# Kernel optimization log

Measured on AMD Instinct MI355X. Metric: run time of the kernel, lower is better.

Reference implementation:

```python
import jax, jax.numpy as jnp
import numpy as np

N = 100000
E = 1600000
D_IN = 256
D_OUT = 128
ALPHA = 0.2  # LeakyReLU negative slope


def setup_inputs() -> dict:
    key = jax.random.key(0)
    k1, k2, k3, k4, k5 = jax.random.split(key, 5)
    x = jax.random.normal(k1, (N, D_IN), dtype=jnp.float32)
    # random edges + self-loops so every destination row has >=1 incoming edge
    src = jax.random.randint(k2, (E - N,), 0, N)
    dst = jax.random.randint(k3, (E - N,), 0, N)
    loops = jnp.arange(N)
    edge = jnp.stack([jnp.concatenate([src, loops]),
                      jnp.concatenate([dst, loops])]).astype(jnp.int64)  # [2, E]
    W = jax.random.normal(k4, (D_IN, D_OUT), dtype=jnp.float32) * 0.1
    a = jax.random.normal(k5, (1, 2 * D_OUT), dtype=jnp.float32) * 0.1
    return {"x": x, "edge": edge, "W": W, "a": a}


def reference(x, edge, W, a):
    n = x.shape[0]
    d_out = W.shape[1]
    h = x @ W  # [n, d_out]
    src, dst = edge[0], edge[1]
    # a @ concat(h[src], h[dst]) decomposes into two per-node projections
    f_src = h @ a[0, :d_out]   # [n]
    f_dst = h @ a[0, d_out:]   # [n]
    tmp = f_src[src] + f_dst[dst]                      # [E]
    lrelu = jnp.where(tmp > 0, tmp, ALPHA * tmp)
    edge_e = jnp.exp(-lrelu)                           # [E]
    # spmm(A, ones) -> rowsum; spmm(A, h) -> weighted aggregation (rows = src)
    e_rowsum = jax.ops.segment_sum(edge_e, src, num_segments=n)           # [n]
    hh = jax.ops.segment_sum(edge_e[:, None] * h[dst], src, num_segments=n)  # [n, d_out]
    hh = hh / e_rowsum[:, None]
    return jax.nn.elu(hh)  # end=False -> apply ELU
```

## Files before the change

### kernel.cpp

```cpp
#include <hip/hip_runtime.h>

#define D_IN 256
#define D_OUT 128
#define ALPHA 0.2f
#define RB 64
#define RBSH 6
#define NBMAX 1600
#define CH 8192
#define CAPG 1536
#define OVFCAP 32768
#define LKH 128
#define BM 64

typedef __attribute__((ext_vector_type(8))) short bf16x8;
typedef __attribute__((ext_vector_type(4))) float f32x4;

__device__ inline unsigned short f2bf(float f) {
    unsigned int u = __float_as_uint(f);
    return (unsigned short)((u + 0x7FFFu + ((u >> 16) & 1u)) >> 16);
}
__device__ inline float bf2f(unsigned short u) {
    return __uint_as_float(((unsigned int)u) << 16);
}
__device__ inline unsigned int cvt_pk_bf16(float lo, float hi) {
    unsigned int r;
    asm("v_cvt_pk_bf16_f32 %0, %1, %2" : "=v"(r) : "v"(lo), "v"(hi));
    return r;
}

__global__ __launch_bounds__(256) void k_wt(const float* __restrict__ W,
                                            unsigned short* __restrict__ WTb) {
    const int ncol = blockIdx.x;
    const int k = threadIdx.x;
    WTb[(size_t)ncol * 256 + k] = f2bf(W[(size_t)k * 128 + ncol]);
}

__global__ __launch_bounds__(256) void k_fused(const float* __restrict__ x,
                                               const unsigned short* __restrict__ WTb,
                                               const float* __restrict__ a,
                                               unsigned short* __restrict__ hb,
                                               float* __restrict__ f_src,
                                               float* __restrict__ f_dst, int n,
                                               const int* __restrict__ src,
                                               const int* __restrict__ dst,
                                               int* __restrict__ gcnt,
                                               int2* __restrict__ ovf,
                                               int* __restrict__ gkeys, int E, int nb,
                                               int nbf) {
    __shared__ char smem[BM * LKH * 2];
    __shared__ float sFp[BM][2][2];
    const int t = threadIdx.x;

    if (blockIdx.x < nbf) {
        int* cnt = (int*)smem;
        int* bas = cnt + NBMAX;
        const int e0 = blockIdx.x * CH;
        const int e1 = min(e0 + CH, E);
        for (int i = t; i < nb; i += 256) cnt[i] = 0;
        __syncthreads();
        for (int e = e0 + t; e < e1; e += 256) atomicAdd(&cnt[src[e] >> RBSH], 1);
        __syncthreads();
        for (int b = t; b < nb; b += 256) {
            int c = cnt[b];
            bas[b] = c ? atomicAdd(&gcnt[b], c) : 0;
            cnt[b] = 0;
        }
        __syncthreads();
        for (int e = e0 + t; e < e1; e += 256) {
            int s = src[e], d = dst[e];
            int b = s >> RBSH;
            int key = ((s & (RB - 1)) << 17) | d;
            int r = bas[b] + atomicAdd(&cnt[b], 1);
            if (r < CAPG) {
                gkeys[b * CAPG + r] = key;
            } else {
                int o = atomicAdd(&gcnt[nb], 1);
                if (o < OVFCAP) ovf[o] = make_int2(b, key);
            }
        }
        return;
    }

    unsigned short* sA = (unsigned short*)smem;
    const int l = t & 63;
    const int w = t >> 6;
    const int wr = w >> 1, wc = w & 1;
    const int row0 = (blockIdx.x - nbf) * BM;
    const int col0 = wc * 64;
    const int lr = l & 15;
    const int g = l >> 4;
    const int lk8 = g * 8;

    f32x4 acc[2][4] = {};
    const unsigned short* bp[4];
    #pragma unroll
    for (int ni = 0; ni < 4; ++ni)
        bp[ni] = WTb + (size_t)(col0 + ni * 16 + lr) * 256 + lk8;

    #pragma unroll
    for (int half = 0; half < 2; ++half) {
        {
            const int rr = t >> 4;
            const int cc = (t & 15) * 8;
            #pragma unroll
            for (int it = 0; it < 4; ++it) {
                int r = it * 16 + rr;
                int gr = row0 + r;
                float4 fa, fb;
                if (gr < n) {
                    const float* xp = &x[(size_t)gr * D_IN + half * LKH + cc];
                    fa = *(const float4*)xp;
                    fb = *(const float4*)(xp + 4);
                } else {
                    fa = make_float4(0.f, 0.f, 0.f, 0.f);
                    fb = fa;
                }
                uint4 v;
                v.x = cvt_pk_bf16(fa.x, fa.y);
                v.y = cvt_pk_bf16(fa.z, fa.w);
                v.z = cvt_pk_bf16(fb.x, fb.y);
                v.w = cvt_pk_bf16(fb.z, fb.w);
                int js = (cc >> 3) ^ ((r & 7) << 1);
                *(uint4*)&sA[r * LKH + js * 8] = v;
            }
        }
        __syncthreads();

        #pragma unroll
        for (int k0 = 0; k0 < LKH; k0 += 32) {
            bf16x8 af[2], bfr[4];
            #pragma unroll
            for (int mi = 0; mi < 2; ++mi) {
                int row_l = wr * 32 + mi * 16 + lr;
                int js = ((k0 >> 3) + g) ^ ((row_l & 7) << 1);
                af[mi] = *(const bf16x8*)&sA[row_l * LKH + js * 8];
            }
            #pragma unroll
            for (int ni = 0; ni < 4; ++ni)
                bfr[ni] = *(const bf16x8*)(bp[ni] + half * LKH + k0);
            #pragma unroll
            for (int mi = 0; mi < 2; ++mi)
                #pragma unroll
                for (int ni = 0; ni < 4; ++ni)
                    acc[mi][ni] = __builtin_amdgcn_mfma_f32_16x16x32_bf16(
                        af[mi], bfr[ni], acc[mi][ni], 0, 0, 0);
        }
        __syncthreads();
    }

    #pragma unroll
    for (int mi = 0; mi < 2; ++mi) {
        #pragma unroll
        for (int q = 0; q < 4; ++q) {
            int r = row0 + wr * 32 + mi * 16 + g * 4 + q;
            if (r < n) {
                unsigned int a01 = cvt_pk_bf16(acc[mi][0][q], acc[mi][1][q]);
                unsigned int a23 = cvt_pk_bf16(acc[mi][2][q], acc[mi][3][q]);
                unsigned short* hp = &hb[(size_t)r * D_OUT + col0 + lr];
                hp[0]  = (unsigned short)(a01 & 0xFFFF);
                hp[16] = (unsigned short)(a01 >> 16);
                hp[32] = (unsigned short)(a23 & 0xFFFF);
                hp[48] = (unsigned short)(a23 >> 16);
            }
        }
    }

    float asv[4], adv[4];
    #pragma unroll
    for (int ni = 0; ni < 4; ++ni) {
        asv[ni] = a[col0 + ni * 16 + lr];
        adv[ni] = a[D_OUT + col0 + ni * 16 + lr];
    }
    #pragma unroll
    for (int mi = 0; mi < 2; ++mi) {
        #pragma unroll
        for (int q = 0; q < 4; ++q) {
            float fs = 0.f, fd = 0.f;
            #pragma unroll
            for (int ni = 0; ni < 4; ++ni) {
                float v = acc[mi][ni][q];
                fs = fmaf(v, asv[ni], fs);
                fd = fmaf(v, adv[ni], fd);
            }
            #pragma unroll
            for (int m = 1; m < 16; m <<= 1) {
                fs += __shfl_xor(fs, m);
                fd += __shfl_xor(fd, m);
            }
            if (lr == 0) {
                int rl = wr * 32 + mi * 16 + g * 4 + q;
                sFp[rl][wc][0] = fs;
                sFp[rl][wc][1] = fd;
            }
        }
    }
    __syncthreads();
    if (t < BM) {
        int r = row0 + t;
        if (r < n) {
            f_src[r] = sFp[t][0][0] + sFp[t][1][0];
            f_dst[r] = sFp[t][0][1] + sFp[t][1][1];
        }
    }
}

__global__ __launch_bounds__(512, 8) void k_bagg(const unsigned short* __restrict__ hb,
                                                 const float* __restrict__ f_src,
                                                 const float* __restrict__ f_dst,
                                                 const int* __restrict__ gcnt,
                                                 const int2* __restrict__ ovf,
                                                 const int* __restrict__ gkeys,
                                                 float* __restrict__ out, int n, int nb) {
    __shared__ int2 sdw[CAPG];
    __shared__ int nbase[RB];
    __shared__ int ncnt[RB];
    __shared__ int ncur[RB];
    __shared__ float fsl[RB];
    __shared__ int sc[RB];
    const int t = threadIdx.x;
    const int b = blockIdx.x;
    const int s0 = b * RB;
    const int nn = min(RB, n - s0);
    const int beg = b * CAPG;
    const int stored = min(gcnt[b], CAPG);
    const int ovf_n = min(gcnt[nb], OVFCAP);

    for (int i = t; i < RB; i += 512) {
        ncnt[i] = 0;
        fsl[i] = (i < nn) ? f_src[s0 + i] : 0.f;
    }
    __syncthreads();

    for (int i = t; i < stored; i += 512)
        atomicAdd(&ncnt[gkeys[beg + i] >> 17], 1);
    __syncthreads();

    if (t < RB) sc[t] = ncnt[t];
    __syncthreads();
    for (int off = 1; off < RB; off <<= 1) {
        int v = 0;
        if (t < RB && t >= off) v = sc[t - off];
        __syncthreads();
        if (t < RB) sc[t] += v;
        __syncthreads();
    }
    if (t < RB) {
        nbase[t] = sc[t] - ncnt[t];
        ncur[t]  = sc[t] - ncnt[t];
    }
    __syncthreads();

    for (int i = t; i < stored; i += 512) {
        int k = gkeys[beg + i];
        int d = k & 0x1FFFF, ls = k >> 17;
        float tmp = fsl[ls] + f_dst[d];
        float w = __expf(-((tmp > 0.f) ? tmp : ALPHA * tmp));
        int pos = atomicAdd(&ncur[ls], 1);
        sdw[pos] = make_int2(d, __float_as_int(w));
    }
    __syncthreads();

    const int lane = t & 63, wid = t >> 6;
    const int cl = (lane & 31) * 4;
    const bool isB = lane >= 32;
    for (int ni = wid; ni < nn; ni += 8) {
        const int jb = nbase[ni];
        const int cn = ncnt[ni];
        const int halfA = (cn + 1) >> 1;
        const int halfB = cn - halfA;
        const int lim = isB ? halfB : halfA;
        const int jbh = jb + (isB ? halfA : 0);
        float a0 = 0.f, a1 = 0.f, a2 = 0.f, a3 = 0.f, rowsum = 0.f;
        #pragma unroll 4
        for (int it = 0; it < halfA; ++it) {
            bool valid = it < lim;
            int2 dw = sdw[valid ? (jbh + it) : jb];
            float w = valid ? __int_as_float(dw.y) : 0.f;
            ushort4 hv = *(const ushort4*)&hb[(size_t)dw.x * D_OUT + cl];
            rowsum += w;
            a0 = fmaf(w, bf2f(hv.x), a0);
            a1 = fmaf(w, bf2f(hv.y), a1);
            a2 = fmaf(w, bf2f(hv.z), a2);
            a3 = fmaf(w, bf2f(hv.w), a3);
        }
        if (ovf_n > 0) {
            for (int o = 0; o < ovf_n; ++o) {
                int2 ov = ovf[o];
                if (ov.x == b && (ov.y >> 17) == ni && !isB) {
                    int d = ov.y & 0x1FFFF;
                    float tmp = fsl[ni] + f_dst[d];
                    float w = __expf(-((tmp > 0.f) ? tmp : ALPHA * tmp));
                    ushort4 hv = *(const ushort4*)&hb[(size_t)d * D_OUT + cl];
                    rowsum += w;
                    a0 = fmaf(w, bf2f(hv.x), a0);
                    a1 = fmaf(w, bf2f(hv.y), a1);
                    a2 = fmaf(w, bf2f(hv.z), a2);
                    a3 = fmaf(w, bf2f(hv.w), a3);
                }
            }
        }
        rowsum += __shfl_xor(rowsum, 32);
        a0 += __shfl_xor(a0, 32);
        a1 += __shfl_xor(a1, 32);
        a2 += __shfl_xor(a2, 32);
        a3 += __shfl_xor(a3, 32);
        if (!isB) {
            float inv = 1.f / rowsum;
            a0 *= inv; a1 *= inv; a2 *= inv; a3 *= inv;
            a0 = (a0 > 0.f) ? a0 : (__expf(a0) - 1.f);
            a1 = (a1 > 0.f) ? a1 : (__expf(a1) - 1.f);
            a2 = (a2 > 0.f) ? a2 : (__expf(a2) - 1.f);
            a3 = (a3 > 0.f) ? a3 : (__expf(a3) - 1.f);
            *(float4*)&out[(size_t)(s0 + ni) * D_OUT + cl] =
                make_float4(a0, a1, a2, a3);
        }
    }
}

extern "C" void kernel_launch(void* const* d_in, const int* in_sizes, int n_in,
                              void* d_out, int out_size, void* d_ws, size_t ws_size,
                              hipStream_t stream) {
    const float* x    = (const float*)d_in[0];
    const int*   edge = (const int*)d_in[1];
    const float* W    = (const float*)d_in[2];
    const float* a    = (const float*)d_in[3];
    float* out = (float*)d_out;

    const int n = in_sizes[0] / D_IN;
    const int E = in_sizes[1] / 2;
    const int* src = edge;
    const int* dst = edge + E;
    const int nb = (n + RB - 1) / RB;

    char* p = (char*)d_ws;
    unsigned short* hb  = (unsigned short*)p; p += (size_t)n * D_OUT * sizeof(unsigned short);
    unsigned short* WTb = (unsigned short*)p; p += (size_t)D_OUT * D_IN * sizeof(unsigned short);
    float* f_src = (float*)p;  p += (size_t)n * sizeof(float);
    float* f_dst = (float*)p;  p += (size_t)n * sizeof(float);
    int*  gcnt   = (int*)p;    p += (size_t)(nb + 1) * sizeof(int);
    int2* ovf    = (int2*)p;   p += (size_t)OVFCAP * sizeof(int2);
    int*  gkeys  = (int*)p;    p += (size_t)nb * CAPG * sizeof(int);

    const int gemm_blocks = (n + BM - 1) / BM;
    const int nbf = (E + CH - 1) / CH;

    hipMemsetAsync(gcnt, 0, (size_t)(nb + 1) * sizeof(int), stream);
    k_wt<<<D_OUT, 256, 0, stream>>>(W, WTb);
    k_fused<<<nbf + gemm_blocks, 256, 0, stream>>>(x, WTb, a, hb, f_src, f_dst, n,
                                                   src, dst, gcnt, ovf, gkeys, E, nb, nbf);
    k_bagg<<<nb, 512, 0, stream>>>(hb, f_src, f_dst, gcnt, ovf, gkeys, out, n, nb);
}
```

Measured before the change: 133.5 us.

## Load x tiles directly to LDS as fp32 and fold gcnt memset into k_wt

The GEMM stage now stages x through LDS with global_load_lds 16-byte direct copies, keeping fp32 in shared memory, and converts to bf16 when MFMA fragments are read. It also drops the separate hipMemsetAsync by zeroing the bucket counters inside block 0 of the weight-transpose kernel. This aims to skip the register round-trip on the x load path and save one launch, but it doubles the LDS tile size and adds conversion work inside the inner MFMA loop.

```diff
diff --git a/kernel.cpp b/kernel.cpp
--- a/kernel.cpp
+++ b/kernel.cpp
@@ -27,9 +27,18 @@
     asm("v_cvt_pk_bf16_f32 %0, %1, %2" : "=v"(r) : "v"(lo), "v"(hi));
     return r;
 }
+__device__ inline void gload_lds16(const float* g, void* lds) {
+    __builtin_amdgcn_global_load_lds(
+        (const __attribute__((address_space(1))) void*)(const void*)g,
+        (__attribute__((address_space(3))) void*)lds, 16, 0, 0);
+}
 
 __global__ __launch_bounds__(256) void k_wt(const float* __restrict__ W,
-                                            unsigned short* __restrict__ WTb) {
+                                            unsigned short* __restrict__ WTb,
+                                            int* __restrict__ gcnt, int nb) {
+    if (blockIdx.x == 0) {
+        for (int i = threadIdx.x; i <= nb; i += 256) gcnt[i] = 0;
+    }
     const int ncol = blockIdx.x;
     const int k = threadIdx.x;
     WTb[(size_t)ncol * 256 + k] = f2bf(W[(size_t)k * 128 + ncol]);
@@ -47,7 +56,7 @@
                                                int2* __restrict__ ovf,
                                                int* __restrict__ gkeys, int E, int nb,
                                                int nbf) {
-    __shared__ char smem[BM * LKH * 2];
+    __shared__ char smem[BM * LKH * 4];
     __shared__ float sFp[BM][2][2];
     const int t = threadIdx.x;
 
@@ -81,7 +90,7 @@
         return;
     }
 
-    unsigned short* sA = (unsigned short*)smem;
+    float* sAf = (float*)smem;
     const int l = t & 63;
     const int w = t >> 6;
     const int wr = w >> 1, wc = w & 1;
@@ -100,28 +109,16 @@
     #pragma unroll
     for (int half = 0; half < 2; ++half) {
         {
-            const int rr = t >> 4;
-            const int cc = (t & 15) * 8;
-            #pragma unroll
-            for (int it = 0; it < 4; ++it) {
-                int r = it * 16 + rr;
+            const int rh = l >> 5;
+            const int gg = l & 31;
+            #pragma unroll
+            for (int it = 0; it < 8; ++it) {
+                int r = w * 16 + it * 2 + rh;
                 int gr = row0 + r;
-                float4 fa, fb;
-                if (gr < n) {
-                    const float* xp = &x[(size_t)gr * D_IN + half * LKH + cc];
-                    fa = *(const float4*)xp;
-                    fb = *(const float4*)(xp + 4);
-                } else {
-                    fa = make_float4(0.f, 0.f, 0.f, 0.f);
-                    fb = fa;
-                }
-                uint4 v;
-                v.x = cvt_pk_bf16(fa.x, fa.y);
-                v.y = cvt_pk_bf16(fa.z, fa.w);
-                v.z = cvt_pk_bf16(fb.x, fb.y);
-                v.w = cvt_pk_bf16(fb.z, fb.w);
-                int js = (cc >> 3) ^ ((r & 7) << 1);
-                *(uint4*)&sA[r * LKH + js * 8] = v;
+                if (gr > n - 1) gr = n - 1;
+                int gs = gg ^ (r & 7);
+                const float* gp = x + (size_t)gr * D_IN + half * LKH + gs * 4;
+                gload_lds16(gp, (char*)smem + (size_t)(w * 16 + it * 2) * 512);
             }
         }
         __syncthreads();
@@ -132,8 +129,17 @@
             #pragma unroll
             for (int mi = 0; mi < 2; ++mi) {
                 int row_l = wr * 32 + mi * 16 + lr;
-                int js = ((k0 >> 3) + g) ^ ((row_l & 7) << 1);
-                af[mi] = *(const bf16x8*)&sA[row_l * LKH + js * 8];
+                int g0 = (k0 >> 2) + g * 2;
+                int gs0 = g0 ^ (row_l & 7);
+                int gs1 = (g0 + 1) ^ (row_l & 7);
+                float4 f0 = *(const float4*)&sAf[(row_l * 32 + gs0) * 4];
+                float4 f1 = *(const float4*)&sAf[(row_l * 32 + gs1) * 4];
+                union { uint4 u; bf16x8 v; } cv;
+                cv.u.x = cvt_pk_bf16(f0.x, f0.y);
+                cv.u.y = cvt_pk_bf16(f0.z, f0.w);
+                cv.u.z = cvt_pk_bf16(f1.x, f1.y);
+                cv.u.w = cvt_pk_bf16(f1.z, f1.w);
+                af[mi] = cv.v;
             }
             #pragma unroll
             for (int ni = 0; ni < 4; ++ni)
@@ -344,8 +350,7 @@
     const int gemm_blocks = (n + BM - 1) / BM;
     const int nbf = (E + CH - 1) / CH;
 
-    hipMemsetAsync(gcnt, 0, (size_t)(nb + 1) * sizeof(int), stream);
-    k_wt<<<D_OUT, 256, 0, stream>>>(W, WTb);
+    k_wt<<<D_OUT, 256, 0, stream>>>(W, WTb, gcnt, nb);
     k_fused<<<nbf + gemm_blocks, 256, 0, stream>>>(x, WTb, a, hb, f_src, f_dst, n,
                                                    src, dst, gcnt, ovf, gkeys, E, nb, nbf);
     k_bagg<<<nb, 512, 0, stream>>>(hb, f_src, f_dst, gcnt, ovf, gkeys, out, n, nb);
```

New measurement: 131.3 us. No clear change (-1.6%).
